# Optimization experiments

Hardware: AMD Instinct MI355X
Metric: run time of the kernel (lower is better)

Reference implementation:

```python
import jax, jax.numpy as jnp
import numpy as np

BS, T, Q, HID, PROJ = 16, 16, 100, 256, 256


def setup_inputs() -> dict:
    key = jax.random.key(0)
    k1, k2, k3, k4, k5 = jax.random.split(key, 5)
    frame_embeds = jax.random.normal(k1, (BS, T, Q, HID), jnp.float32)
    other_frame_embeds = jax.random.normal(k2, (BS, T, Q, HID), jnp.float32)
    W = jax.random.normal(k3, (HID, PROJ), jnp.float32) / np.sqrt(HID).astype(np.float32)
    b = jax.random.normal(k4, (PROJ,), jnp.float32) * 0.01
    n = BS * Q
    mid = jax.random.randint(k5, (n, 1), 1, T - 1, dtype=jnp.int32)
    bridge = jnp.concatenate(
        [jnp.zeros((n, 1), jnp.int32), mid, jnp.full((n, 1), T - 1, jnp.int32)], axis=1
    )  # (n,3): head=0, random pivot in [1,T-2], tail=T-1
    return {"frame_embeds": frame_embeds, "other_frame_embeds": other_frame_embeds,
            "W": W, "b": b, "bridge": bridge}


def _prep(fe, W, b):
    # Linear proj, (bs,t,q,c)->(bs*q, t, c), L2-normalize per embedding.
    bs, t, q, _ = fe.shape
    x = fe @ W + b
    x = x.transpose(0, 2, 1, 3).reshape(bs * q, t, -1)
    return x / jnp.linalg.norm(x, axis=-1, keepdims=True)


def _forward(frame_embeds, other_frame_embeds, W, b, bridge, delta=0.3):
    cur = _prep(frame_embeds, W, b)      # (n,t,c)
    other = _prep(other_frame_embeds, W, b)
    bh = bridge[:, 0].astype(jnp.float32)
    bp_f = bridge[:, 1].astype(jnp.float32)
    bt = bridge[:, 2].astype(jnp.float32)
    alpha = (bp_f - bh) / (bt - bh)      # (n,)
    sigma = alpha * (bt - bp_f)          # (n,)
    g = jnp.take_along_axis(cur, bridge[:, :, None], axis=1)  # (n,3,c) head/pivot/tail
    # positive brownian-bridge distance
    x = g[:, 1] - (1.0 - alpha)[:, None] * g[:, 0] - alpha[:, None] * g[:, 2]
    numer = jnp.exp(-jnp.sum(x * x, axis=-1) / (2.0 * sigma ** 2))  # (n,)
    # negatives: pivot frame taken from every sequence in [cur; other].
    # ||m_ij - a_i||^2 = ||m_ij||^2 - 2 m_ij.a_i + ||a_i||^2 with m_ij = neg_all[j, bp_i],
    # avoiding the (n,N,3,c) repeat tensor of the original.
    neg_all = jnp.concatenate([cur, other], axis=0)            # (N,t,c)
    a = (1.0 - alpha)[:, None] * g[:, 0] + alpha[:, None] * g[:, 2]  # (n,c)
    cross = jnp.einsum('ic,jtc->ijt', a, neg_all)              # (n,N,t)
    bp = bridge[:, 1]
    cross_g = jnp.take_along_axis(cross, bp[:, None, None], axis=2)[..., 0]  # (n,N)
    nn2_g = jnp.sum(neg_all * neg_all, axis=-1).T[bp]          # (n,N)
    x2 = nn2_g - 2.0 * cross_g + jnp.sum(a * a, axis=-1)[:, None]
    dist = -x2 / (2.0 * sigma ** 2)[:, None]                   # (n,N)
    n = dist.shape[0]
    idx = jnp.arange(n)
    self_dist = dist[idx, idx]
    dist = dist.at[idx, idx].set(-10000.0)
    topv, _ = jax.lax.top_k(dist, 5)
    deno = jnp.exp(jnp.concatenate([self_dist[:, None], topv], axis=-1))  # (n,6)
    brownian_loss = (numer / deno.sum(axis=-1)).mean()
    score = jnp.einsum('nc,nc->n', cur[:, 0], cur[:, -1])
    head_tail_match = jax.nn.softplus(delta - score).mean()
    return brownian_loss, head_tail_match


def reference(frame_embeds, other_frame_embeds, W, b, bridge):
    return _forward(frame_embeds, other_frame_embeds, W, b, bridge)
```

## Files before the change

kernel.cpp:

```cpp
#include <hip/hip_runtime.h>
#include <hip/hip_bf16.h>

#define NROW 1600
#define NEG  3200
#define ROWS_FLAT 25600
#define NSPLIT 25

using bf16x8 = __attribute__((ext_vector_type(8))) short;
using f32x4  = __attribute__((ext_vector_type(4))) float;

__device__ __forceinline__ float bf2f(unsigned v) { return __uint_as_float(v << 16); }
__device__ __forceinline__ ushort f2bf(float f) {
  __hip_bfloat16 h = __float2bfloat16(f);
  return *(ushort*)&h;
}
__device__ __forceinline__ float load1(const ushort* p, size_t idx, int f32) {
  return f32 ? ((const float*)p)[idx] : bf2f(p[idx]);
}
__device__ __forceinline__ void load8(const ushort* p, size_t idx, int f32, float* o) {
  if (f32) {
    const float* q = (const float*)p;
    float4 a = *(const float4*)(q + idx);
    float4 b = *(const float4*)(q + idx + 4);
    o[0]=a.x; o[1]=a.y; o[2]=a.z; o[3]=a.w;
    o[4]=b.x; o[5]=b.y; o[6]=b.z; o[7]=b.w;
  } else {
    uint4 u = *(const uint4*)(p + idx);
    o[0]=bf2f(u.x & 0xffffu); o[1]=bf2f(u.x >> 16);
    o[2]=bf2f(u.y & 0xffffu); o[3]=bf2f(u.y >> 16);
    o[4]=bf2f(u.z & 0xffffu); o[5]=bf2f(u.z >> 16);
    o[6]=bf2f(u.w & 0xffffu); o[7]=bf2f(u.w >> 16);
  }
}
__device__ __forceinline__ int sniff_f32(const ushort* p, int lane) {
  unsigned e = ((unsigned)p[2*lane] >> 7) & 0xffu;
  unsigned long long b = __ballot(e >= 100u && e <= 140u);
  return (__popcll(b) >= 40) ? 0 : 1;
}

__global__ __launch_bounds__(256) void k_prepw(const ushort* __restrict__ W,
    ushort* __restrict__ Wt, int* __restrict__ zbase) {
  if (blockIdx.x == 0 && threadIdx.x < 21) zbase[threadIdx.x] = 0;
  int fW = sniff_f32(W, threadIdx.x & 63);
  int n = blockIdx.x, k = threadIdx.x;
  Wt[n*256 + k] = f2bf(load1(W, (size_t)k*256 + n, fW));
}

__global__ __launch_bounds__(256) void k_proj(const ushort* __restrict__ fe0,
    const ushort* __restrict__ fe1, const ushort* __restrict__ Wt,
    const ushort* __restrict__ bias, ushort* __restrict__ Pb) {
  __shared__ union {
    ushort x[64*256];
    ushort c[4][32*72];
  } sh;
  __shared__ float s_ss[4][64];
  const int tid = threadIdx.x;
  const int w = tid >> 6, lane = tid & 63, q = lane >> 4, m = lane & 15;
  const int grow0 = blockIdx.x * 64;
  const int src1 = (grow0 >= ROWS_FLAT);
  const ushort* src = src1 ? fe1 : fe0;
  const size_t rbase = (size_t)(src1 ? grow0 - ROWS_FLAT : grow0) * 256;
  const int fSrc = sniff_f32(src, lane);
  const int fB   = sniff_f32(bias, lane);
  if (!fSrc) {
    #pragma unroll
    for (int i = 0; i < 8; i++) {
      int l = tid + i*256;
      int r = l >> 5, kc = l & 31;
      uint4 u = *(const uint4*)(src + rbase + (size_t)r*256 + kc*8);
      *(uint4*)&sh.x[r*256 + ((kc*8) ^ ((r&7)<<3))] = u;
    }
  } else {
    #pragma unroll
    for (int i = 0; i < 8; i++) {
      int l = tid + i*256;
      int r = l >> 5, kc = l & 31;
      float o[8];
      load8(src, rbase + (size_t)r*256 + kc*8, 1, o);
      uint4 u;
      u.x = (unsigned)f2bf(o[0]) | ((unsigned)f2bf(o[1]) << 16);
      u.y = (unsigned)f2bf(o[2]) | ((unsigned)f2bf(o[3]) << 16);
      u.z = (unsigned)f2bf(o[4]) | ((unsigned)f2bf(o[5]) << 16);
      u.w = (unsigned)f2bf(o[6]) | ((unsigned)f2bf(o[7]) << 16);
      *(uint4*)&sh.x[r*256 + ((kc*8) ^ ((r&7)<<3))] = u;
    }
  }
  __syncthreads();
  f32x4 acc[4][4];
  #pragma unroll
  for (int nt = 0; nt < 4; nt++) {
    float bb = load1(bias, w*64 + nt*16 + m, fB);
    f32x4 v = {bb, bb, bb, bb};
    #pragma unroll
    for (int mt = 0; mt < 4; mt++) acc[mt][nt] = v;
  }
  const int sw = (m & 7) << 3;
  const ushort* wbase = Wt + (size_t)(w*64 + m)*256 + q*8;
  bf16x8 a_cur[4], b_cur[4];
  #pragma unroll
  for (int mt = 0; mt < 4; mt++)
    a_cur[mt] = *(const bf16x8*)&sh.x[(mt*16 + m)*256 + ((q*8) ^ sw)];
  #pragma unroll
  for (int nt = 0; nt < 4; nt++)
    b_cur[nt] = *(const bf16x8*)(wbase + (size_t)nt*16*256);
  #pragma unroll
  for (int k = 0; k < 8; k++) {
    bf16x8 a_nxt[4], b_nxt[4];
    if (k < 7) {
      int k0 = (k + 1) * 32;
      #pragma unroll
      for (int nt = 0; nt < 4; nt++)
        b_nxt[nt] = *(const bf16x8*)(wbase + (size_t)nt*16*256 + k0);
      int pk = (k0 + q*8) ^ sw;
      #pragma unroll
      for (int mt = 0; mt < 4; mt++)
        a_nxt[mt] = *(const bf16x8*)&sh.x[(mt*16 + m)*256 + pk];
    }
    #pragma unroll
    for (int nt = 0; nt < 4; nt++)
      #pragma unroll
      for (int mt = 0; mt < 4; mt++)
        acc[mt][nt] = __builtin_amdgcn_mfma_f32_16x16x32_bf16(a_cur[mt], b_cur[nt], acc[mt][nt], 0, 0, 0);
    if (k < 7) {
      #pragma unroll
      for (int x = 0; x < 4; x++) { a_cur[x] = a_nxt[x]; b_cur[x] = b_nxt[x]; }
    }
  }
  float ssp[4][4];
  #pragma unroll
  for (int mt = 0; mt < 4; mt++)
    #pragma unroll
    for (int reg = 0; reg < 4; reg++) {
      float s = 0.f;
      #pragma unroll
      for (int nt = 0; nt < 4; nt++) { float v = acc[mt][nt][reg]; s += v*v; }
      ssp[mt][reg] = s;
    }
  #pragma unroll
  for (int mk = 1; mk < 16; mk <<= 1)
    #pragma unroll
    for (int mt = 0; mt < 4; mt++)
      #pragma unroll
      for (int reg = 0; reg < 4; reg++) ssp[mt][reg] += __shfl_xor(ssp[mt][reg], mk, 64);
  if (m == 0)
    #pragma unroll
    for (int mt = 0; mt < 4; mt++)
      #pragma unroll
      for (int reg = 0; reg < 4; reg++) s_ss[w][mt*16 + 4*q + reg] = ssp[mt][reg];
  __syncthreads();
  float inv[4][4];
  #pragma unroll
  for (int mt = 0; mt < 4; mt++)
    #pragma unroll
    for (int reg = 0; reg < 4; reg++) {
      int row = mt*16 + 4*q + reg;
      float s = s_ss[0][row] + s_ss[1][row] + s_ss[2][row] + s_ss[3][row];
      inv[mt][reg] = 1.0f / sqrtf(s);
    }
  #pragma unroll
  for (int half = 0; half < 2; half++) {
    #pragma unroll
    for (int mt = half*2; mt < half*2 + 2; mt++)
      #pragma unroll
      for (int reg = 0; reg < 4; reg++) {
        int rl = (mt - half*2)*16 + 4*q + reg;
        #pragma unroll
        for (int nt = 0; nt < 4; nt++)
          sh.c[w][rl*72 + nt*16 + m] = f2bf(acc[mt][nt][reg] * inv[mt][reg]);
      }
    int rl = (lane >> 3), c16 = lane & 7;
    #pragma unroll
    for (int it = 0; it < 4; it++) {
      int row = it*8 + rl;
      int grow = grow0 + half*32 + row;
      int srcid = grow / ROWS_FLAT;
      int rem   = grow % ROWS_FLAT;
      int b  = rem / 1600;
      int t  = (rem / 100) & 15;
      int qq = rem % 100;
      size_t orow = ((size_t)(srcid*1600 + b*100 + qq) * 16 + t) * 256;
      uint4 v = *(uint4*)&sh.c[w][row*72 + c16*8];
      *(uint4*)(Pb + orow + w*64 + c16*8) = v;
    }
  }
}

__global__ __launch_bounds__(256) void k_bridge(const ushort* __restrict__ Pb,
    const int* __restrict__ bridge, ushort* __restrict__ Ab,
    float* __restrict__ prm, float* __restrict__ numer,
    int* __restrict__ cnt, int* __restrict__ lst, float* __restrict__ wsum) {
  int i = blockIdx.x, c = threadIdx.x;
  int bh = bridge[i*3+0], bp = bridge[i*3+1], bt = bridge[i*3+2];
  float bhf = (float)bh, bpf = (float)bp, btf = (float)bt;
  float alpha = (bpf - bhf) / (btf - bhf);
  float sigma = alpha * (btf - bpf);
  const ushort* base = Pb + (size_t)i * 16 * 256;
  float g0 = bf2f(base[bh*256 + c]), g1 = bf2f(base[bp*256 + c]), g2 = bf2f(base[bt*256 + c]);
  float head = bf2f(base[c]), tail = bf2f(base[15*256 + c]);
  float a = (1.0f - alpha) * g0 + alpha * g2;
  float x = g1 - a;
  Ab[(size_t)i*256 + c] = f2bf(a);
  float xx = x*x, aac = a*a, sc = head*tail;
  #pragma unroll
  for (int mk = 1; mk < 64; mk <<= 1) {
    xx  += __shfl_xor(xx, mk, 64);
    aac += __shfl_xor(aac, mk, 64);
    sc  += __shfl_xor(sc, mk, 64);
  }
  __shared__ float red[3][4];
  int wv = c >> 6;
  if ((c & 63) == 0) { red[0][wv]=xx; red[1][wv]=aac; red[2][wv]=sc; }
  __syncthreads();
  if (c == 0) {
    float XX = red[0][0]+red[0][1]+red[0][2]+red[0][3];
    float AA = red[1][0]+red[1][1]+red[1][2]+red[1][3];
    float SC = red[2][0]+red[2][1]+red[2][2]+red[2][3];
    float inv2s2 = 1.0f / (2.0f * sigma * sigma);
    prm[i*2+0] = inv2s2;
    prm[i*2+1] = AA;
    numer[i] = expf(-XX * inv2s2);
    float sp = log1pf(expf(0.3f - SC));
    atomicAdd(wsum + 1, sp * (1.0f / 1600.0f));
    int pos = atomicAdd(cnt + bp, 1);
    lst[bp * 1600 + pos] = i;
  }
}

__device__ __forceinline__ void sort5(float* c) {
  #define CE(i,j) { float hi = fmaxf(c[i], c[j]), lo = fminf(c[i], c[j]); c[i]=hi; c[j]=lo; }
  CE(0,1) CE(3,4) CE(2,4) CE(2,3) CE(1,4) CE(0,3) CE(0,2) CE(1,3) CE(1,2)
  #undef CE
}
__device__ __forceinline__ void ins5(float* t, float v) {
  float hi, lo;
  hi = fmaxf(t[0], v); lo = fminf(t[0], v); t[0] = hi; v = lo;
  hi = fmaxf(t[1], v); lo = fminf(t[1], v); t[1] = hi; v = lo;
  hi = fmaxf(t[2], v); lo = fminf(t[2], v); t[2] = hi; v = lo;
  hi = fmaxf(t[3], v); lo = fminf(t[3], v); t[3] = hi; v = lo;
  t[4] = fmaxf(t[4], v);
}

__global__ __launch_bounds__(256) void k_cross(const ushort* __restrict__ Pb,
    const ushort* __restrict__ Ab, const float* __restrict__ prm,
    const int* __restrict__ cnt, const int* __restrict__ lst,
    float* __restrict__ part) {
  int t = blockIdx.z;
  int n_t = min(cnt[t], 1600);
  int i0 = blockIdx.y * 32;
  if (i0 >= n_t) return;
  int j0 = blockIdx.x * 128;
  __shared__ int s_gis[32];
  __shared__ float s_red[4][32][6];
  int tid = threadIdx.x;
  if (tid < 32) {
    int gi = lst[t*1600 + min(i0 + tid, n_t - 1)];
    s_gis[tid] = min(max(gi, 0), NROW - 1);
  }
  __syncthreads();
  const int w = tid >> 6, lane = tid & 63, q = lane >> 4, m = lane & 15;
  const ushort* jp0 = Pb + ((size_t)(j0 + w*32 + m)*16 + t) * 256 + q*8;
  const ushort* jp1 = jp0 + (size_t)16*16*256;
  int gi0 = s_gis[m], gi1 = s_gis[16 + m];
  const ushort* ip0 = Ab + (size_t)gi0 * 256 + q*8;
  const ushort* ip1 = Ab + (size_t)gi1 * 256 + q*8;
  f32x4 acc[2][2];
  #pragma unroll
  for (int jt = 0; jt < 2; jt++)
    #pragma unroll
    for (int it = 0; it < 2; it++) { f32x4 z = {0.f,0.f,0.f,0.f}; acc[jt][it] = z; }
  bf16x8 jc0 = *(const bf16x8*)(jp0);
  bf16x8 jc1 = *(const bf16x8*)(jp1);
  bf16x8 ic0 = *(const bf16x8*)(ip0);
  bf16x8 ic1 = *(const bf16x8*)(ip1);
  #pragma unroll
  for (int k = 0; k < 8; k++) {
    bf16x8 jn0, jn1, in0, in1;
    if (k < 7) {
      int o = (k + 1) * 32;
      jn0 = *(const bf16x8*)(jp0 + o);
      jn1 = *(const bf16x8*)(jp1 + o);
      in0 = *(const bf16x8*)(ip0 + o);
      in1 = *(const bf16x8*)(ip1 + o);
    }
    acc[0][0] = __builtin_amdgcn_mfma_f32_16x16x32_bf16(jc0, ic0, acc[0][0], 0, 0, 0);
    acc[0][1] = __builtin_amdgcn_mfma_f32_16x16x32_bf16(jc0, ic1, acc[0][1], 0, 0, 0);
    acc[1][0] = __builtin_amdgcn_mfma_f32_16x16x32_bf16(jc1, ic0, acc[1][0], 0, 0, 0);
    acc[1][1] = __builtin_amdgcn_mfma_f32_16x16x32_bf16(jc1, ic1, acc[1][1], 0, 0, 0);
    if (k < 7) { jc0 = jn0; jc1 = jn1; ic0 = in0; ic1 = in1; }
  }
  float top[2][5], selfv[2] = {-1e30f, -1e30f};
  float p0i = prm[gi0*2], p0a = prm[gi0*2+1];
  float p1i = prm[gi1*2], p1a = prm[gi1*2+1];
  #pragma unroll
  for (int it = 0; it < 2; it++)
    #pragma unroll
    for (int k = 0; k < 5; k++) top[it][k] = -1e30f;
  #pragma unroll
  for (int jt = 0; jt < 2; jt++)
    #pragma unroll
    for (int reg = 0; reg < 4; reg++) {
      int j = j0 + w*32 + jt*16 + 4*q + reg;
      float d0 = -(1.0f - 2.0f*acc[jt][0][reg] + p0a) * p0i;
      float d1 = -(1.0f - 2.0f*acc[jt][1][reg] + p1a) * p1i;
      if (j == gi0) selfv[0] = d0; else ins5(top[0], d0);
      if (j == gi1) selfv[1] = d1; else ins5(top[1], d1);
    }
  #pragma unroll
  for (int mk = 16; mk <= 32; mk <<= 1) {
    #pragma unroll
    for (int it = 0; it < 2; it++) {
      float o[5], c[5];
      #pragma unroll
      for (int k = 0; k < 5; k++) o[k] = __shfl_xor(top[it][k], mk, 64);
      #pragma unroll
      for (int k = 0; k < 5; k++) c[k] = fmaxf(top[it][k], o[4 - k]);
      sort5(c);
      #pragma unroll
      for (int k = 0; k < 5; k++) top[it][k] = c[k];
      selfv[it] = fmaxf(selfv[it], __shfl_xor(selfv[it], mk, 64));
    }
  }
  if (q == 0) {
    #pragma unroll
    for (int it = 0; it < 2; it++) {
      #pragma unroll
      for (int k = 0; k < 5; k++) s_red[w][it*16 + m][k] = top[it][k];
      s_red[w][it*16 + m][5] = selfv[it];
    }
  }
  __syncthreads();
  if (tid < 32 && i0 + tid < n_t) {
    float T[5], S = s_red[0][tid][5];
    #pragma unroll
    for (int k = 0; k < 5; k++) T[k] = s_red[0][tid][k];
    #pragma unroll
    for (int w2 = 1; w2 < 4; w2++) {
      #pragma unroll
      for (int k = 0; k < 5; k++) ins5(T, s_red[w2][tid][k]);
      S = fmaxf(S, s_red[w2][tid][5]);
    }
    float* pp = part + ((size_t)s_gis[tid]*NSPLIT + blockIdx.x) * 6;
    #pragma unroll
    for (int k = 0; k < 5; k++) pp[k] = T[k];
    pp[5] = S;
  }
}

__global__ __launch_bounds__(64) void k_merge(const float* __restrict__ part,
    const float* __restrict__ numer, float* __restrict__ wsum, int* __restrict__ done,
    const ushort* __restrict__ fe0, void* __restrict__ out) {
  int i = blockIdx.x * 64 + threadIdx.x;
  const float* pp = part + (size_t)i * NSPLIT * 6;
  float T[5]; float S = pp[5];
  #pragma unroll
  for (int k = 0; k < 5; k++) T[k] = pp[k];
  #pragma unroll
  for (int s = 1; s < NSPLIT; s++) {
    const float* ps = pp + s*6;
    float v0 = ps[0], v1 = ps[1], v2 = ps[2], v3 = ps[3], v4 = ps[4], v5 = ps[5];
    ins5(T, v0); ins5(T, v1); ins5(T, v2); ins5(T, v3); ins5(T, v4);
    S = fmaxf(S, v5);
  }
  float deno = expf(S);
  #pragma unroll
  for (int k = 0; k < 5; k++) deno += expf(T[k]);
  float local = numer[i] / deno;
  #pragma unroll
  for (int mk = 1; mk < 64; mk <<= 1) local += __shfl_xor(local, mk, 64);
  __shared__ int s_last;
  if (threadIdx.x == 0) {
    atomicAdd(wsum + 0, local * (1.0f / 1600.0f));
    __threadfence();
    s_last = (atomicAdd(done, 1) == 24);
  }
  __syncthreads();
  if (s_last) {
    int f = sniff_f32(fe0, threadIdx.x);
    if (threadIdx.x == 0) {
      __threadfence();
      float brown = __hip_atomic_load(wsum + 0, __ATOMIC_RELAXED, __HIP_MEMORY_SCOPE_AGENT);
      float sp    = __hip_atomic_load(wsum + 1, __ATOMIC_RELAXED, __HIP_MEMORY_SCOPE_AGENT);
      if (f) {
        ((float*)out)[0] = brown;
        ((float*)out)[1] = sp;
      } else {
        ushort* o = (ushort*)out;
        o[0] = f2bf(brown);
        o[1] = f2bf(sp);
      }
    }
  }
}

extern "C" void kernel_launch(void* const* d_in, const int* in_sizes, int n_in,
                              void* d_out, int out_size, void* d_ws, size_t ws_size,
                              hipStream_t stream) {
  const ushort* fe0    = (const ushort*)d_in[0];
  const ushort* fe1    = (const ushort*)d_in[1];
  const ushort* W      = (const ushort*)d_in[2];
  const ushort* bias   = (const ushort*)d_in[3];
  const int*    bridge = (const int*)d_in[4];

  ushort* Pb    = (ushort*)d_ws;
  ushort* Ab    = Pb + 13107200;
  ushort* Wt    = Ab + 409600;
  float*  part  = (float*)(Wt + 65536);
  float*  prm   = part + 240000;
  float*  numer = prm + 3200;
  float*  wsum  = numer + 1600;
  int*    cnt   = (int*)(wsum + 4);
  int*    done  = cnt + 16;
  int*    lst   = done + 1;

  k_prepw <<<256, 256, 0, stream>>>(W, Wt, (int*)wsum);
  k_proj  <<<800, 256, 0, stream>>>(fe0, fe1, Wt, bias, Pb);
  k_bridge<<<1600, 256, 0, stream>>>(Pb, bridge, Ab, prm, numer, cnt, lst, wsum);
  k_cross <<<dim3(NSPLIT, 13, 16), 256, 0, stream>>>(Pb, Ab, prm, cnt, lst, part);
  k_merge <<<25, 64, 0, stream>>>(part, numer, wsum, done, fe0, d_out);
}
```

Before: 191.7 us.

## Load projection A-operand directly from global and widen cross-kernel i-tile to 64

The projection kernel stops staging the input tile in shared memory and feeds MFMA A-operands straight from global (converting fp32 to bf16 on the fly), removing the LDS store, barrier and swizzled reads. Separately, the cross kernel processes 64 query rows per block instead of 32, so each loaded j-tile of negatives is reused across twice as many queries and the grid shrinks. The trade-offs are redundant global reads of A across the four waves in the projection kernel and higher register pressure in the cross kernel.

```diff
diff --git a/kernel.cpp b/kernel.cpp
--- a/kernel.cpp
+++ b/kernel.cpp
@@ -17,20 +17,17 @@
 __device__ __forceinline__ float load1(const ushort* p, size_t idx, int f32) {
   return f32 ? ((const float*)p)[idx] : bf2f(p[idx]);
 }
-__device__ __forceinline__ void load8(const ushort* p, size_t idx, int f32, float* o) {
-  if (f32) {
-    const float* q = (const float*)p;
-    float4 a = *(const float4*)(q + idx);
-    float4 b = *(const float4*)(q + idx + 4);
-    o[0]=a.x; o[1]=a.y; o[2]=a.z; o[3]=a.w;
-    o[4]=b.x; o[5]=b.y; o[6]=b.z; o[7]=b.w;
-  } else {
-    uint4 u = *(const uint4*)(p + idx);
-    o[0]=bf2f(u.x & 0xffffu); o[1]=bf2f(u.x >> 16);
-    o[2]=bf2f(u.y & 0xffffu); o[3]=bf2f(u.y >> 16);
-    o[4]=bf2f(u.z & 0xffffu); o[5]=bf2f(u.z >> 16);
-    o[6]=bf2f(u.w & 0xffffu); o[7]=bf2f(u.w >> 16);
-  }
+__device__ __forceinline__ bf16x8 load8bf(const ushort* p, size_t idx, int f32) {
+  if (!f32) return *(const bf16x8*)(p + idx);
+  const float* q = (const float*)p;
+  float4 a = *(const float4*)(q + idx);
+  float4 b = *(const float4*)(q + idx + 4);
+  uint4 u;
+  u.x = (unsigned)f2bf(a.x) | ((unsigned)f2bf(a.y) << 16);
+  u.y = (unsigned)f2bf(a.z) | ((unsigned)f2bf(a.w) << 16);
+  u.z = (unsigned)f2bf(b.x) | ((unsigned)f2bf(b.y) << 16);
+  u.w = (unsigned)f2bf(b.z) | ((unsigned)f2bf(b.w) << 16);
+  return *(bf16x8*)&u;
 }
 __device__ __forceinline__ int sniff_f32(const ushort* p, int lane) {
   unsigned e = ((unsigned)p[2*lane] >> 7) & 0xffu;
@@ -49,10 +46,7 @@
 __global__ __launch_bounds__(256) void k_proj(const ushort* __restrict__ fe0,
     const ushort* __restrict__ fe1, const ushort* __restrict__ Wt,
     const ushort* __restrict__ bias, ushort* __restrict__ Pb) {
-  __shared__ union {
-    ushort x[64*256];
-    ushort c[4][32*72];
-  } sh;
+  __shared__ ushort shc[4][32*72];
   __shared__ float s_ss[4][64];
   const int tid = threadIdx.x;
   const int w = tid >> 6, lane = tid & 63, q = lane >> 4, m = lane & 15;
@@ -62,30 +56,6 @@
   const size_t rbase = (size_t)(src1 ? grow0 - ROWS_FLAT : grow0) * 256;
   const int fSrc = sniff_f32(src, lane);
   const int fB   = sniff_f32(bias, lane);
-  if (!fSrc) {
-    #pragma unroll
-    for (int i = 0; i < 8; i++) {
-      int l = tid + i*256;
-      int r = l >> 5, kc = l & 31;
-      uint4 u = *(const uint4*)(src + rbase + (size_t)r*256 + kc*8);
-      *(uint4*)&sh.x[r*256 + ((kc*8) ^ ((r&7)<<3))] = u;
-    }
-  } else {
-    #pragma unroll
-    for (int i = 0; i < 8; i++) {
-      int l = tid + i*256;
-      int r = l >> 5, kc = l & 31;
-      float o[8];
-      load8(src, rbase + (size_t)r*256 + kc*8, 1, o);
-      uint4 u;
-      u.x = (unsigned)f2bf(o[0]) | ((unsigned)f2bf(o[1]) << 16);
-      u.y = (unsigned)f2bf(o[2]) | ((unsigned)f2bf(o[3]) << 16);
-      u.z = (unsigned)f2bf(o[4]) | ((unsigned)f2bf(o[5]) << 16);
-      u.w = (unsigned)f2bf(o[6]) | ((unsigned)f2bf(o[7]) << 16);
-      *(uint4*)&sh.x[r*256 + ((kc*8) ^ ((r&7)<<3))] = u;
-    }
-  }
-  __syncthreads();
   f32x4 acc[4][4];
   #pragma unroll
   for (int nt = 0; nt < 4; nt++) {
@@ -94,12 +64,12 @@
     #pragma unroll
     for (int mt = 0; mt < 4; mt++) acc[mt][nt] = v;
   }
-  const int sw = (m & 7) << 3;
   const ushort* wbase = Wt + (size_t)(w*64 + m)*256 + q*8;
+  const size_t abase = rbase + (size_t)m*256 + q*8;
   bf16x8 a_cur[4], b_cur[4];
   #pragma unroll
   for (int mt = 0; mt < 4; mt++)
-    a_cur[mt] = *(const bf16x8*)&sh.x[(mt*16 + m)*256 + ((q*8) ^ sw)];
+    a_cur[mt] = load8bf(src, abase + (size_t)mt*16*256, fSrc);
   #pragma unroll
   for (int nt = 0; nt < 4; nt++)
     b_cur[nt] = *(const bf16x8*)(wbase + (size_t)nt*16*256);
@@ -111,10 +81,9 @@
       #pragma unroll
       for (int nt = 0; nt < 4; nt++)
         b_nxt[nt] = *(const bf16x8*)(wbase + (size_t)nt*16*256 + k0);
-      int pk = (k0 + q*8) ^ sw;
       #pragma unroll
       for (int mt = 0; mt < 4; mt++)
-        a_nxt[mt] = *(const bf16x8*)&sh.x[(mt*16 + m)*256 + pk];
+        a_nxt[mt] = load8bf(src, abase + (size_t)mt*16*256 + k0, fSrc);
     }
     #pragma unroll
     for (int nt = 0; nt < 4; nt++)
@@ -166,7 +135,7 @@
         int rl = (mt - half*2)*16 + 4*q + reg;
         #pragma unroll
         for (int nt = 0; nt < 4; nt++)
-          sh.c[w][rl*72 + nt*16 + m] = f2bf(acc[mt][nt][reg] * inv[mt][reg]);
+          shc[w][rl*72 + nt*16 + m] = f2bf(acc[mt][nt][reg] * inv[mt][reg]);
       }
     int rl = (lane >> 3), c16 = lane & 7;
     #pragma unroll
@@ -179,7 +148,7 @@
       int t  = (rem / 100) & 15;
       int qq = rem % 100;
       size_t orow = ((size_t)(srcid*1600 + b*100 + qq) * 16 + t) * 256;
-      uint4 v = *(uint4*)&sh.c[w][row*72 + c16*8];
+      uint4 v = *(uint4*)&shc[w][row*72 + c16*8];
       *(uint4*)(Pb + orow + w*64 + c16*8) = v;
     }
   }
@@ -246,13 +215,13 @@
     float* __restrict__ part) {
   int t = blockIdx.z;
   int n_t = min(cnt[t], 1600);
-  int i0 = blockIdx.y * 32;
+  int i0 = blockIdx.y * 64;
   if (i0 >= n_t) return;
   int j0 = blockIdx.x * 128;
-  __shared__ int s_gis[32];
-  __shared__ float s_red[4][32][6];
+  __shared__ int s_gis[64];
+  __shared__ float s_red[4][64][6];
   int tid = threadIdx.x;
-  if (tid < 32) {
+  if (tid < 64) {
     int gi = lst[t*1600 + min(i0 + tid, n_t - 1)];
     s_gis[tid] = min(max(gi, 0), NROW - 1);
   }
@@ -260,55 +229,67 @@
   const int w = tid >> 6, lane = tid & 63, q = lane >> 4, m = lane & 15;
   const ushort* jp0 = Pb + ((size_t)(j0 + w*32 + m)*16 + t) * 256 + q*8;
   const ushort* jp1 = jp0 + (size_t)16*16*256;
-  int gi0 = s_gis[m], gi1 = s_gis[16 + m];
-  const ushort* ip0 = Ab + (size_t)gi0 * 256 + q*8;
-  const ushort* ip1 = Ab + (size_t)gi1 * 256 + q*8;
-  f32x4 acc[2][2];
+  int gi[4];
+  const ushort* ip[4];
+  #pragma unroll
+  for (int it = 0; it < 4; it++) {
+    gi[it] = s_gis[it*16 + m];
+    ip[it] = Ab + (size_t)gi[it] * 256 + q*8;
+  }
+  f32x4 acc[2][4];
   #pragma unroll
   for (int jt = 0; jt < 2; jt++)
     #pragma unroll
-    for (int it = 0; it < 2; it++) { f32x4 z = {0.f,0.f,0.f,0.f}; acc[jt][it] = z; }
+    for (int it = 0; it < 4; it++) { f32x4 z = {0.f,0.f,0.f,0.f}; acc[jt][it] = z; }
   bf16x8 jc0 = *(const bf16x8*)(jp0);
   bf16x8 jc1 = *(const bf16x8*)(jp1);
-  bf16x8 ic0 = *(const bf16x8*)(ip0);
-  bf16x8 ic1 = *(const bf16x8*)(ip1);
+  bf16x8 ic[4];
+  #pragma unroll
+  for (int it = 0; it < 4; it++) ic[it] = *(const bf16x8*)(ip[it]);
   #pragma unroll
   for (int k = 0; k < 8; k++) {
-    bf16x8 jn0, jn1, in0, in1;
+    bf16x8 jn0, jn1, in[4];
     if (k < 7) {
       int o = (k + 1) * 32;
       jn0 = *(const bf16x8*)(jp0 + o);
       jn1 = *(const bf16x8*)(jp1 + o);
-      in0 = *(const bf16x8*)(ip0 + o);
-      in1 = *(const bf16x8*)(ip1 + o);
-    }
-    acc[0][0] = __builtin_amdgcn_mfma_f32_16x16x32_bf16(jc0, ic0, acc[0][0], 0, 0, 0);
-    acc[0][1] = __builtin_amdgcn_mfma_f32_16x16x32_bf16(jc0, ic1, acc[0][1], 0, 0, 0);
-    acc[1][0] = __builtin_amdgcn_mfma_f32_16x16x32_bf16(jc1, ic0, acc[1][0], 0, 0, 0);
-    acc[1][1] = __builtin_amdgcn_mfma_f32_16x16x32_bf16(jc1, ic1, acc[1][1], 0, 0, 0);
-    if (k < 7) { jc0 = jn0; jc1 = jn1; ic0 = in0; ic1 = in1; }
-  }
-  float top[2][5], selfv[2] = {-1e30f, -1e30f};
-  float p0i = prm[gi0*2], p0a = prm[gi0*2+1];
-  float p1i = prm[gi1*2], p1a = prm[gi1*2+1];
-  #pragma unroll
-  for (int it = 0; it < 2; it++)
+      #pragma unroll
+      for (int it = 0; it < 4; it++) in[it] = *(const bf16x8*)(ip[it] + o);
+    }
+    #pragma unroll
+    for (int it = 0; it < 4; it++) {
+      acc[0][it] = __builtin_amdgcn_mfma_f32_16x16x32_bf16(jc0, ic[it], acc[0][it], 0, 0, 0);
+      acc[1][it] = __builtin_amdgcn_mfma_f32_16x16x32_bf16(jc1, ic[it], acc[1][it], 0, 0, 0);
+    }
+    if (k < 7) { jc0 = jn0; jc1 = jn1;
+      #pragma unroll
+      for (int it = 0; it < 4; it++) ic[it] = in[it];
+    }
+  }
+  float top[4][5], selfv[4];
+  float pi[4], pa[4];
+  #pragma unroll
+  for (int it = 0; it < 4; it++) {
+    pi[it] = prm[gi[it]*2]; pa[it] = prm[gi[it]*2+1];
+    selfv[it] = -1e30f;
     #pragma unroll
     for (int k = 0; k < 5; k++) top[it][k] = -1e30f;
+  }
   #pragma unroll
   for (int jt = 0; jt < 2; jt++)
     #pragma unroll
     for (int reg = 0; reg < 4; reg++) {
       int j = j0 + w*32 + jt*16 + 4*q + reg;
-      float d0 = -(1.0f - 2.0f*acc[jt][0][reg] + p0a) * p0i;
-      float d1 = -(1.0f - 2.0f*acc[jt][1][reg] + p1a) * p1i;
-      if (j == gi0) selfv[0] = d0; else ins5(top[0], d0);
-      if (j == gi1) selfv[1] = d1; else ins5(top[1], d1);
+      #pragma unroll
+      for (int it = 0; it < 4; it++) {
+        float d = -(1.0f - 2.0f*acc[jt][it][reg] + pa[it]) * pi[it];
+        if (j == gi[it]) selfv[it] = d; else ins5(top[it], d);
+      }
     }
   #pragma unroll
   for (int mk = 16; mk <= 32; mk <<= 1) {
     #pragma unroll
-    for (int it = 0; it < 2; it++) {
+    for (int it = 0; it < 4; it++) {
       float o[5], c[5];
       #pragma unroll
       for (int k = 0; k < 5; k++) o[k] = __shfl_xor(top[it][k], mk, 64);
@@ -322,14 +303,14 @@
   }
   if (q == 0) {
     #pragma unroll
-    for (int it = 0; it < 2; it++) {
+    for (int it = 0; it < 4; it++) {
       #pragma unroll
       for (int k = 0; k < 5; k++) s_red[w][it*16 + m][k] = top[it][k];
       s_red[w][it*16 + m][5] = selfv[it];
     }
   }
   __syncthreads();
-  if (tid < 32 && i0 + tid < n_t) {
+  if (tid < 64 && i0 + tid < n_t) {
     float T[5], S = s_red[0][tid][5];
     #pragma unroll
     for (int k = 0; k < 5; k++) T[k] = s_red[0][tid][k];
@@ -415,6 +396,6 @@
   k_prepw <<<256, 256, 0, stream>>>(W, Wt, (int*)wsum);
   k_proj  <<<800, 256, 0, stream>>>(fe0, fe1, Wt, bias, Pb);
   k_bridge<<<1600, 256, 0, stream>>>(Pb, bridge, Ab, prm, numer, cnt, lst, wsum);
-  k_cross <<<dim3(NSPLIT, 13, 16), 256, 0, stream>>>(Pb, Ab, prm, cnt, lst, part);
+  k_cross <<<dim3(NSPLIT, 7, 16), 256, 0, stream>>>(Pb, Ab, prm, cnt, lst, part);
   k_merge <<<25, 64, 0, stream>>>(part, numer, wsum, done, fe0, d_out);
 }
```

Result: slower. 209.9 us (+9.5%).
